# Kernel tuning notes

Measured on AMD Instinct MI355X. Metric: run time of the kernel, lower is better.

Reference implementation:

```python
import jax, jax.numpy as jnp
import numpy as np

N, IN_DIM, OUT_DIM, HEADS = 50000, 128, 32, 8
E = 800000
F = OUT_DIM * HEADS  # 256 fused output features
SEM_HID = 128        # SemanticAttention hidden size (HAN default)


def setup_inputs() -> dict:
    key = jax.random.key(0)
    ks = jax.random.split(key, 16)
    inp = {
        "h": jax.random.normal(ks[0], (N, IN_DIM), jnp.float32),
        "src_a": jax.random.randint(ks[1], (E,), 0, N, jnp.int32),
        "dst_a": jax.random.randint(ks[2], (E,), 0, N, jnp.int32),
        "src_b": jax.random.randint(ks[3], (E,), 0, N, jnp.int32),
        "dst_b": jax.random.randint(ks[4], (E,), 0, N, jnp.int32),
    }
    s = 1.0 / np.sqrt(IN_DIM)
    # per-metapath GATConv params
    inp["W_a"] = jax.random.normal(ks[5], (IN_DIM, F), jnp.float32) * s
    inp["al_a"] = jax.random.normal(ks[6], (HEADS, OUT_DIM), jnp.float32) * 0.1
    inp["ar_a"] = jax.random.normal(ks[7], (HEADS, OUT_DIM), jnp.float32) * 0.1
    inp["bias_a"] = jnp.zeros((F,), jnp.float32)
    inp["W_b"] = jax.random.normal(ks[8], (IN_DIM, F), jnp.float32) * s
    inp["al_b"] = jax.random.normal(ks[9], (HEADS, OUT_DIM), jnp.float32) * 0.1
    inp["ar_b"] = jax.random.normal(ks[10], (HEADS, OUT_DIM), jnp.float32) * 0.1
    inp["bias_b"] = jnp.zeros((F,), jnp.float32)
    # semantic attention params
    inp["Wsem"] = jax.random.normal(ks[11], (F, SEM_HID), jnp.float32) / np.sqrt(F)
    inp["bsem"] = jnp.zeros((SEM_HID,), jnp.float32)
    inp["wsem"] = jax.random.normal(ks[12], (SEM_HID,), jnp.float32) / np.sqrt(SEM_HID)
    return inp


def gat_conv(h, src, dst, W, al, ar, bias):
    # h: [N, in_dim] -> feat: [N, H, D]
    feat = (h @ W).reshape(N, HEADS, OUT_DIM)
    el = (feat * al).sum(-1)  # [N, H]
    er = (feat * ar).sum(-1)  # [N, H]
    e = jax.nn.leaky_relu(el[src] + er[dst], 0.2)  # [E, H]
    # edge softmax over incoming edges of each dst node (numerically stable)
    m = jax.ops.segment_max(e, dst, num_segments=N)        # -inf for empty
    ex = jnp.exp(e - m[dst])                               # [E, H]
    denom = jax.ops.segment_sum(ex, dst, num_segments=N)   # [N, H]
    msg = feat[src] * ex[:, :, None]                       # [E, H, D]
    out = jax.ops.segment_sum(msg, dst, num_segments=N)    # [N, H, D]
    out = out / jnp.where(denom > 0, denom, 1.0)[:, :, None]
    return jax.nn.elu(out.reshape(N, F) + bias)


def reference(h, src_a, dst_a, src_b, dst_b,
              W_a, al_a, ar_a, bias_a,
              W_b, al_b, ar_b, bias_b,
              Wsem, bsem, wsem):
    z_a = gat_conv(h, src_a, dst_a, W_a, al_a, ar_a, bias_a)
    z_b = gat_conv(h, src_b, dst_b, W_b, al_b, ar_b, bias_b)
    z = jnp.stack([z_a, z_b], axis=1)                 # [N, M, F]
    q = jnp.tanh(z @ Wsem + bsem) @ wsem              # [N, M]
    beta = jax.nn.softmax(q.mean(axis=0))             # [M]
    return (z * beta[None, :, None]).sum(axis=1)      # [N, F]
```

## Files before the change

kernel.cpp:

```cpp
#include <hip/hip_runtime.h>
#include <stdint.h>

#define NN 50000
#define EE 800000
#define IN_DIM 128
#define OUT_DIM 32
#define HEADS 8
#define FF 256
#define SH 128
#define NPAD 50048
#define FEXT 272
#define CAP 64

#define RANK_G   6250
#define A_WSEMT0 6250
#define A_BTA0   (A_WSEMT0 + 128)
#define A_BTB0   (A_BTA0 + FEXT)
#define A_G      (A_BTB0 + FEXT)

#define GEMM_BLKS 782
#define B_G      (2 * GEMM_BLKS)

#define PULL_G   12500
#define C_G      (2 * PULL_G)
#define D_G      (2 * GEMM_BLKS)

typedef short s16x8 __attribute__((ext_vector_type(8)));
typedef float f32x4 __attribute__((ext_vector_type(4)));

__device__ __forceinline__ float b2f(unsigned short u) {
    union { unsigned int i; float f; } v; v.i = ((unsigned int)u) << 16; return v.f;
}
__device__ __forceinline__ unsigned short f2b(float f) {
    union { float f; unsigned int i; } v; v.f = f;
    unsigned int i = v.i;
    unsigned int r = (i + 0x7FFFu + ((i >> 16) & 1u)) >> 16;
    return (unsigned short)r;
}

__device__ __forceinline__ void buildBT_one(
    const float* __restrict__ W, const float* __restrict__ al,
    const float* __restrict__ ar, unsigned short* __restrict__ BT,
    int fp, int k)
{
    float v;
    if (fp < FF) {
        v = W[(size_t)k * FF + fp];
    } else if (fp < FF + 8) {
        int hh = fp - FF;
        float s = 0.f;
        #pragma unroll
        for (int d = 0; d < 32; ++d) s += W[(size_t)k * FF + hh * 32 + d] * al[hh * 32 + d];
        v = s;
    } else {
        int hh = fp - FF - 8;
        float s = 0.f;
        #pragma unroll
        for (int d = 0; d < 32; ++d) s += W[(size_t)k * FF + hh * 32 + d] * ar[hh * 32 + d];
        v = s;
    }
    BT[(size_t)fp * IN_DIM + k] = f2b(v);
}

__global__ __launch_bounds__(256) void megaA(
    const int* __restrict__ src_a, const int* __restrict__ dst_a,
    const int* __restrict__ src_b, const int* __restrict__ dst_b,
    int* __restrict__ counts_a, int* __restrict__ counts_b,
    unsigned short* __restrict__ perm_a, unsigned short* __restrict__ perm_b,
    const float* __restrict__ Wsem, unsigned short* __restrict__ WsemT,
    const float* __restrict__ W_a, const float* __restrict__ al_a,
    const float* __restrict__ ar_a, unsigned short* __restrict__ BT_a,
    const float* __restrict__ W_b, const float* __restrict__ al_b,
    const float* __restrict__ ar_b, unsigned short* __restrict__ BT_b)
{
    int b = blockIdx.x, t = threadIdx.x;
    if (b < RANK_G) {
        int idx = b * 256 + t;
        if (idx < EE) {
            int d = dst_a[idx];
            int r = atomicAdd(&counts_a[d], 1);
            perm_a[d * CAP + r] = (unsigned short)src_a[idx];
        } else {
            int e = idx - EE;
            int d = dst_b[e];
            int r = atomicAdd(&counts_b[d], 1);
            perm_b[d * CAP + r] = (unsigned short)src_b[e];
        }
    } else if (b < A_BTA0) {
        int j = b - A_WSEMT0;
        WsemT[j * FF + t] = f2b(Wsem[(size_t)t * SH + j]);
    } else if (b < A_BTB0) {
        if (t < IN_DIM) buildBT_one(W_a, al_a, ar_a, BT_a, b - A_BTA0, t);
    } else {
        if (t < IN_DIM) buildBT_one(W_b, al_b, ar_b, BT_b, b - A_BTB0, t);
    }
}

__global__ __launch_bounds__(256) void megaB(
    const float* __restrict__ h,
    const unsigned short* __restrict__ BT_a, const unsigned short* __restrict__ BT_b,
    unsigned short* __restrict__ feat_a, unsigned short* __restrict__ feat_b,
    float* __restrict__ el_a, float* __restrict__ er_a,
    float* __restrict__ el_b, float* __restrict__ er_b)
{
    int g = blockIdx.x, t = threadIdx.x;
    int mp = (g >= GEMM_BLKS);
    int gb = mp ? g - GEMM_BLKS : g;
    const unsigned short* BT = mp ? BT_b : BT_a;
    unsigned short* feat = mp ? feat_b : feat_a;
    float* el = mp ? el_b : el_a;
    float* er = mp ? er_b : er_a;

    int wave = t >> 6, lane = t & 63;
    int quad = lane >> 4, l16 = lane & 15;
    int nbase = gb * 64 + wave * 16;
    int n = nbase + l16;
    int nr = (n < NN) ? n : (NN - 1);
    const float* hrow = h + (size_t)nr * IN_DIM + quad * 8;
    s16x8 nfr[4];
    #pragma unroll
    for (int kt = 0; kt < 4; ++kt) {
        float4 p0 = *(const float4*)(hrow + kt * 32);
        float4 p1 = *(const float4*)(hrow + kt * 32 + 4);
        s16x8 v;
        v[0] = (short)f2b(p0.x); v[1] = (short)f2b(p0.y);
        v[2] = (short)f2b(p0.z); v[3] = (short)f2b(p0.w);
        v[4] = (short)f2b(p1.x); v[5] = (short)f2b(p1.y);
        v[6] = (short)f2b(p1.z); v[7] = (short)f2b(p1.w);
        nfr[kt] = v;
    }
    bool live = (n < NN);
    #pragma unroll 1
    for (int ft = 0; ft < 17; ++ft) {
        const unsigned short* brow = BT + (size_t)(ft * 16 + l16) * IN_DIM + quad * 8;
        f32x4 c = {0.f, 0.f, 0.f, 0.f};
        #pragma unroll
        for (int kt = 0; kt < 4; ++kt) {
            s16x8 ffr = *(const s16x8*)(brow + kt * 32);
            c = __builtin_amdgcn_mfma_f32_16x16x32_bf16(ffr, nfr[kt], c, 0, 0, 0);
        }
        if (ft < 16) {
            if (live) {
                ushort4 r;
                r.x = f2b(c[0]); r.y = f2b(c[1]); r.z = f2b(c[2]); r.w = f2b(c[3]);
                *(ushort4*)(feat + (size_t)n * FF + ft * 16 + quad * 4) = r;
            }
        } else if (live) {
            #pragma unroll
            for (int r = 0; r < 4; ++r) {
                int jp = quad * 4 + r;
                if (jp < 8) el[n * HEADS + jp] = c[r];
                else        er[n * HEADS + (jp - 8)] = c[r];
            }
        }
    }
}

__global__ __launch_bounds__(256) void megaC(
    const int* __restrict__ counts_a, const int* __restrict__ counts_b,
    const unsigned short* __restrict__ perm_a, const unsigned short* __restrict__ perm_b,
    const float* __restrict__ el_a, const float* __restrict__ er_a,
    const float* __restrict__ el_b, const float* __restrict__ er_b,
    const unsigned short* __restrict__ feat_a, const unsigned short* __restrict__ feat_b,
    const float* __restrict__ bias_a, const float* __restrict__ bias_b,
    unsigned short* __restrict__ zb_a, unsigned short* __restrict__ zb_b)
{
    int bb = blockIdx.x;
    int mp = (bb >= PULL_G);
    int blk = mp ? bb - PULL_G : bb;
    const int* counts = mp ? counts_b : counts_a;
    const unsigned short* perm = mp ? perm_b : perm_a;
    const float* el = mp ? el_b : el_a;
    const float* er = mp ? er_b : er_a;
    const unsigned short* feat = mp ? feat_b : feat_a;
    const float* bias = mp ? bias_b : bias_a;
    unsigned short* zb = mp ? zb_b : zb_a;

    int wave = threadIdx.x >> 6;
    int lane = threadIdx.x & 63;
    int n = blk * 4 + wave;
    int sub = lane >> 5;
    int l32 = lane & 31;
    int head = l32 >> 2;
    int fbase = l32 * 8;
    int deg = counts[n];
    int base = n * CAP;
    float ern = er[n * HEADS + head];
    float den = 0.f;
    float acc[8];
    #pragma unroll
    for (int u = 0; u < 8; ++u) acc[u] = 0.f;

#define STEP(S) {                                                    \
        float x = el[(S) * HEADS + head] + ern;                      \
        x = fmaxf(x, 0.2f * x);                                      \
        float ex = __expf(x);                                        \
        den += ex;                                                   \
        uint4 fv = *(const uint4*)(feat + (size_t)(S) * FF + fbase); \
        const unsigned short* fp = (const unsigned short*)&fv;       \
        acc[0] += b2f(fp[0]) * ex; acc[1] += b2f(fp[1]) * ex;        \
        acc[2] += b2f(fp[2]) * ex; acc[3] += b2f(fp[3]) * ex;        \
        acc[4] += b2f(fp[4]) * ex; acc[5] += b2f(fp[5]) * ex;        \
        acc[6] += b2f(fp[6]) * ex; acc[7] += b2f(fp[7]) * ex; }

    int jp = sub;
    for (; jp + 2 < deg; jp += 4) {
        int s0 = perm[base + jp];
        int s1 = perm[base + jp + 2];
        STEP(s0); STEP(s1);
    }
    if (jp < deg) {
        int s0 = perm[base + jp];
        STEP(s0);
    }
#undef STEP

    den += __shfl_xor(den, 32, 64);
    #pragma unroll
    for (int u = 0; u < 8; ++u) acc[u] += __shfl_xor(acc[u], 32, 64);

    if (den <= 0.f) den = 1.f;
    float inv = 1.f / den;
    float4 b0 = *(const float4*)(bias + fbase);
    float4 b1 = *(const float4*)(bias + fbase + 4);
    float bv[8] = {b0.x, b0.y, b0.z, b0.w, b1.x, b1.y, b1.z, b1.w};
    if (sub == 0) {
        ushort4 r0, r1;
        unsigned short rr[8];
        #pragma unroll
        for (int u = 0; u < 8; ++u) {
            float ov = acc[u] * inv + bv[u];
            ov = (ov > 0.f) ? ov : (__expf(ov) - 1.f);
            rr[u] = f2b(ov);
        }
        r0.x = rr[0]; r0.y = rr[1]; r0.z = rr[2]; r0.w = rr[3];
        r1.x = rr[4]; r1.y = rr[5]; r1.z = rr[6]; r1.w = rr[7];
        *(ushort4*)(zb + (size_t)n * FF + fbase) = r0;
        *(ushort4*)(zb + (size_t)n * FF + fbase + 4) = r1;
    }
}

__global__ __launch_bounds__(256) void megaD(
    const unsigned short* __restrict__ zb_a, const unsigned short* __restrict__ zb_b,
    const unsigned short* __restrict__ WsemT,
    const float* __restrict__ bsem, const float* __restrict__ wsem,
    float* __restrict__ qsum)
{
    int bb = blockIdx.x;
    int mp = (bb >= GEMM_BLKS);
    int blk = mp ? bb - GEMM_BLKS : bb;
    const unsigned short* zb = mp ? zb_b : zb_a;

    int wave = threadIdx.x >> 6, lane = threadIdx.x & 63;
    int quad = lane >> 4, l16 = lane & 15;
    int nbase = blk * 64 + wave * 16;
    const unsigned short* arow = zb + (size_t)(nbase + l16) * FF + quad * 8;
    s16x8 afr[8];
    #pragma unroll
    for (int kt = 0; kt < 8; ++kt)
        afr[kt] = *(const s16x8*)(arow + kt * 32);
    float qacc = 0.f;
    for (int jt = 0; jt < 8; ++jt) {
        int jj = jt * 16 + l16;
        const unsigned short* brow = WsemT + (size_t)jj * FF + quad * 8;
        f32x4 c = {0.f, 0.f, 0.f, 0.f};
        #pragma unroll
        for (int kt = 0; kt < 8; ++kt) {
            s16x8 bfr = *(const s16x8*)(brow + kt * 32);
            c = __builtin_amdgcn_mfma_f32_16x16x32_bf16(afr[kt], bfr, c, 0, 0, 0);
        }
        float bj = bsem[jj], wj = wsem[jj];
        #pragma unroll
        for (int r = 0; r < 4; ++r) {
            int n = nbase + quad * 4 + r;
            float tv = tanhf(c[r] + bj) * wj;
            qacc += (n < NN) ? tv : 0.f;
        }
    }
    #pragma unroll
    for (int o = 1; o < 64; o <<= 1) qacc += __shfl_xor(qacc, o, 64);
    __shared__ float wsum[4];
    if (lane == 0) wsum[wave] = qacc;
    __syncthreads();
    if (threadIdx.x == 0)
        atomicAdd(&qsum[mp], wsum[0] + wsum[1] + wsum[2] + wsum[3]);
}

__global__ __launch_bounds__(256) void combine_kernel(
    const unsigned short* __restrict__ za,
    const unsigned short* __restrict__ zbm,
    float* __restrict__ out, const float* __restrict__ qsum)
{
    size_t i = (size_t)blockIdx.x * blockDim.x + threadIdx.x;
    size_t base = i * 4;
    if (base >= (size_t)NN * FF) return;
    float qa = qsum[0] * (1.f / NN), qb = qsum[1] * (1.f / NN);
    float mx = fmaxf(qa, qb);
    float ea = __expf(qa - mx), eb = __expf(qb - mx);
    float inv = 1.f / (ea + eb);
    float b0 = ea * inv, b1 = eb * inv;
    ushort4 va = *(const ushort4*)(za + base);
    ushort4 vb = *(const ushort4*)(zbm + base);
    float4 r;
    r.x = b0 * b2f(va.x) + b1 * b2f(vb.x);
    r.y = b0 * b2f(va.y) + b1 * b2f(vb.y);
    r.z = b0 * b2f(va.z) + b1 * b2f(vb.z);
    r.w = b0 * b2f(va.w) + b1 * b2f(vb.w);
    *(float4*)(out + base) = r;
}

extern "C" void kernel_launch(void* const* d_in, const int* in_sizes, int n_in,
                              void* d_out, int out_size, void* d_ws, size_t ws_size,
                              hipStream_t stream)
{
    const float* h      = (const float*)d_in[0];
    const int* src_a    = (const int*)d_in[1];
    const int* dst_a    = (const int*)d_in[2];
    const int* src_b    = (const int*)d_in[3];
    const int* dst_b    = (const int*)d_in[4];
    const float* W_a    = (const float*)d_in[5];
    const float* al_a   = (const float*)d_in[6];
    const float* ar_a   = (const float*)d_in[7];
    const float* bias_a = (const float*)d_in[8];
    const float* W_b    = (const float*)d_in[9];
    const float* al_b   = (const float*)d_in[10];
    const float* ar_b   = (const float*)d_in[11];
    const float* bias_b = (const float*)d_in[12];
    const float* Wsem   = (const float*)d_in[13];
    const float* bsem   = (const float*)d_in[14];
    const float* wsem   = (const float*)d_in[15];
    float* out = (float*)d_out;

    char* ws = (char*)d_ws;
    size_t o = 0;
    auto alloc = [&](size_t bytes) -> char* {
        char* p = ws + o;
        o += (bytes + 255) & ~(size_t)255;
        return p;
    };
    unsigned short* BT_a   = (unsigned short*)alloc((size_t)FEXT * IN_DIM * 2);
    unsigned short* BT_b   = (unsigned short*)alloc((size_t)FEXT * IN_DIM * 2);
    unsigned short* feat_a = (unsigned short*)alloc((size_t)NN * FF * 2);
    unsigned short* feat_b = (unsigned short*)alloc((size_t)NN * FF * 2);
    unsigned short* zb_a   = (unsigned short*)alloc((size_t)NPAD * FF * 2);
    unsigned short* zb_b   = (unsigned short*)alloc((size_t)NPAD * FF * 2);
    unsigned short* WsemT  = (unsigned short*)alloc((size_t)SH * FF * 2);
    float* el_a    = (float*)alloc((size_t)NN * HEADS * 4);
    float* er_a    = (float*)alloc((size_t)NN * HEADS * 4);
    float* el_b    = (float*)alloc((size_t)NN * HEADS * 4);
    float* er_b    = (float*)alloc((size_t)NN * HEADS * 4);
    unsigned short* perm_a = (unsigned short*)alloc((size_t)NN * CAP * 2);
    unsigned short* perm_b = (unsigned short*)alloc((size_t)NN * CAP * 2);
    char* zspan0   = ws + o;
    int* counts_a  = (int*)alloc((size_t)NN * 4);
    int* counts_b  = (int*)alloc((size_t)NN * 4);
    float* qsum    = (float*)alloc(8);
    size_t zspan   = (size_t)((ws + o) - zspan0);

    hipMemsetAsync(zspan0, 0, zspan, stream);
    megaA<<<A_G, 256, 0, stream>>>(src_a, dst_a, src_b, dst_b,
                                   counts_a, counts_b, perm_a, perm_b,
                                   Wsem, WsemT,
                                   W_a, al_a, ar_a, BT_a,
                                   W_b, al_b, ar_b, BT_b);
    megaB<<<B_G, 256, 0, stream>>>(h, BT_a, BT_b, feat_a, feat_b,
                                   el_a, er_a, el_b, er_b);
    megaC<<<C_G, 256, 0, stream>>>(counts_a, counts_b, perm_a, perm_b,
                                   el_a, er_a, el_b, er_b,
                                   feat_a, feat_b, bias_a, bias_b, zb_a, zb_b);
    megaD<<<D_G, 256, 0, stream>>>(zb_a, zb_b, WsemT, bsem, wsem, qsum);
    combine_kernel<<<(int)(((size_t)NN * FF / 4 + 255) / 256), 256, 0, stream>>>(zb_a, zb_b, out, qsum);
}
```

Baseline: 494.1 us.

## Split edge bucketing into rank atomics and a scatter pass fused with GEMM

The atomic counting pass now only records each edge's rank within its destination bucket. The scatter of source indices into the per-destination perm table moves into the GEMM kernel as extra blocks, which also clamp writes to CAP. The aim is to shorten the latency-bound atomic kernel and overlap the scattered perm writes with the feature GEMM. In exchange it adds a rank buffer, a second pass over dst/src, and caps degree at CAP in the pull kernel.

```diff
diff --git a/kernel.cpp b/kernel.cpp
--- a/kernel.cpp
+++ b/kernel.cpp
@@ -18,8 +18,9 @@
 #define A_BTB0   (A_BTA0 + FEXT)
 #define A_G      (A_BTB0 + FEXT)
 
+#define B_FILL   6250
 #define GEMM_BLKS 782
-#define B_G      (2 * GEMM_BLKS)
+#define B_G      (B_FILL + 2 * GEMM_BLKS)
 
 #define PULL_G   12500
 #define C_G      (2 * PULL_G)
@@ -63,10 +64,9 @@
 }
 
 __global__ __launch_bounds__(256) void megaA(
-    const int* __restrict__ src_a, const int* __restrict__ dst_a,
-    const int* __restrict__ src_b, const int* __restrict__ dst_b,
+    const int* __restrict__ dst_a, const int* __restrict__ dst_b,
     int* __restrict__ counts_a, int* __restrict__ counts_b,
-    unsigned short* __restrict__ perm_a, unsigned short* __restrict__ perm_b,
+    unsigned short* __restrict__ rank_a, unsigned short* __restrict__ rank_b,
     const float* __restrict__ Wsem, unsigned short* __restrict__ WsemT,
     const float* __restrict__ W_a, const float* __restrict__ al_a,
     const float* __restrict__ ar_a, unsigned short* __restrict__ BT_a,
@@ -77,14 +77,10 @@
     if (b < RANK_G) {
         int idx = b * 256 + t;
         if (idx < EE) {
-            int d = dst_a[idx];
-            int r = atomicAdd(&counts_a[d], 1);
-            perm_a[d * CAP + r] = (unsigned short)src_a[idx];
+            rank_a[idx] = (unsigned short)atomicAdd(&counts_a[dst_a[idx]], 1);
         } else {
             int e = idx - EE;
-            int d = dst_b[e];
-            int r = atomicAdd(&counts_b[d], 1);
-            perm_b[d * CAP + r] = (unsigned short)src_b[e];
+            rank_b[e] = (unsigned short)atomicAdd(&counts_b[dst_b[e]], 1);
         }
     } else if (b < A_BTA0) {
         int j = b - A_WSEMT0;
@@ -97,13 +93,30 @@
 }
 
 __global__ __launch_bounds__(256) void megaB(
+    const int* __restrict__ src_a, const int* __restrict__ dst_a,
+    const int* __restrict__ src_b, const int* __restrict__ dst_b,
+    const unsigned short* __restrict__ rank_a, const unsigned short* __restrict__ rank_b,
+    unsigned short* __restrict__ perm_a, unsigned short* __restrict__ perm_b,
     const float* __restrict__ h,
     const unsigned short* __restrict__ BT_a, const unsigned short* __restrict__ BT_b,
     unsigned short* __restrict__ feat_a, unsigned short* __restrict__ feat_b,
     float* __restrict__ el_a, float* __restrict__ er_a,
     float* __restrict__ el_b, float* __restrict__ er_b)
 {
-    int g = blockIdx.x, t = threadIdx.x;
+    int b = blockIdx.x, t = threadIdx.x;
+    if (b < B_FILL) {
+        int idx = b * 256 + t;
+        if (idx < EE) {
+            int r = rank_a[idx];
+            if (r < CAP) perm_a[dst_a[idx] * CAP + r] = (unsigned short)src_a[idx];
+        } else {
+            int e = idx - EE;
+            int r = rank_b[e];
+            if (r < CAP) perm_b[dst_b[e] * CAP + r] = (unsigned short)src_b[e];
+        }
+        return;
+    }
+    int g = b - B_FILL;
     int mp = (g >= GEMM_BLKS);
     int gb = mp ? g - GEMM_BLKS : g;
     const unsigned short* BT = mp ? BT_b : BT_a;
@@ -184,6 +197,7 @@
     int head = l32 >> 2;
     int fbase = l32 * 8;
     int deg = counts[n];
+    if (deg > CAP) deg = CAP;
     int base = n * CAP;
     float ern = er[n * HEADS + head];
     float den = 0.f;
@@ -349,6 +363,8 @@
     float* er_a    = (float*)alloc((size_t)NN * HEADS * 4);
     float* el_b    = (float*)alloc((size_t)NN * HEADS * 4);
     float* er_b    = (float*)alloc((size_t)NN * HEADS * 4);
+    unsigned short* rank_a = (unsigned short*)alloc((size_t)EE * 2);
+    unsigned short* rank_b = (unsigned short*)alloc((size_t)EE * 2);
     unsigned short* perm_a = (unsigned short*)alloc((size_t)NN * CAP * 2);
     unsigned short* perm_b = (unsigned short*)alloc((size_t)NN * CAP * 2);
     char* zspan0   = ws + o;
@@ -358,12 +374,13 @@
     size_t zspan   = (size_t)((ws + o) - zspan0);
 
     hipMemsetAsync(zspan0, 0, zspan, stream);
-    megaA<<<A_G, 256, 0, stream>>>(src_a, dst_a, src_b, dst_b,
-                                   counts_a, counts_b, perm_a, perm_b,
+    megaA<<<A_G, 256, 0, stream>>>(dst_a, dst_b, counts_a, counts_b, rank_a, rank_b,
                                    Wsem, WsemT,
                                    W_a, al_a, ar_a, BT_a,
                                    W_b, al_b, ar_b, BT_b);
-    megaB<<<B_G, 256, 0, stream>>>(h, BT_a, BT_b, feat_a, feat_b,
+    megaB<<<B_G, 256, 0, stream>>>(src_a, dst_a, src_b, dst_b,
+                                   rank_a, rank_b, perm_a, perm_b,
+                                   h, BT_a, BT_b, feat_a, feat_b,
                                    el_a, er_a, el_b, er_b);
     megaC<<<C_G, 256, 0, stream>>>(counts_a, counts_b, perm_a, perm_b,
                                    el_a, er_a, el_b, er_b,
```

Measured after the change: 471.1 us. 4.7% less time.

## Fuse pipeline stages into one cooperative persistent kernel with grid syncs

Applied to the files above, without the earlier changes.

Replaces the chain of separate launches (rank/prep, GEMM, pull, semantic, combine) with a single cooperative kernel of 1024 persistent blocks that loops over virtual blocks and uses grid.sync between phases. The edge bucketing now runs concurrently with the GEMM phase, and bucket overflow is guarded by clamping to CAP. The aim is to remove launch gaps and kernel-boundary drains, at the cost of grid-wide barrier overhead, a fixed grid size that may under-occupy phases, and reduced latency hiding in the memory-bound pull phase. A non-cooperative multi-kernel fallback is kept.

```diff
diff --git a/kernel.cpp b/kernel.cpp
--- a/kernel.cpp
+++ b/kernel.cpp
@@ -1,8 +1,12 @@
 #include <hip/hip_runtime.h>
+#include <hip/hip_cooperative_groups.h>
 #include <stdint.h>
+
+namespace cg = cooperative_groups;
 
 #define NN 50000
 #define EE 800000
+#define EHALF 400000
 #define IN_DIM 128
 #define OUT_DIM 32
 #define HEADS 8
@@ -12,18 +16,11 @@
 #define FEXT 272
 #define CAP 64
 
-#define RANK_G   6250
-#define A_WSEMT0 6250
-#define A_BTA0   (A_WSEMT0 + 128)
-#define A_BTB0   (A_BTA0 + FEXT)
-#define A_G      (A_BTB0 + FEXT)
-
+#define CGRID 1024
+#define RANKC 1563
 #define GEMM_BLKS 782
-#define B_G      (2 * GEMM_BLKS)
-
-#define PULL_G   12500
-#define C_G      (2 * PULL_G)
-#define D_G      (2 * GEMM_BLKS)
+#define PULL_G 12500
+#define PREP_V 672
 
 typedef short s16x8 __attribute__((ext_vector_type(8)));
 typedef float f32x4 __attribute__((ext_vector_type(4)));
@@ -37,6 +34,20 @@
     unsigned int r = (i + 0x7FFFu + ((i >> 16) & 1u)) >> 16;
     return (unsigned short)r;
 }
+
+struct KParams {
+    const int *src_a, *dst_a, *src_b, *dst_b;
+    const float *h;
+    const float *W_a, *al_a, *ar_a, *bias_a;
+    const float *W_b, *al_b, *ar_b, *bias_b;
+    const float *Wsem, *bsem, *wsem;
+    float* out;
+    unsigned short *BT_a, *BT_b, *feat_a, *feat_b, *zb_a, *zb_b, *WsemT;
+    float *el_a, *er_a, *el_b, *er_b;
+    unsigned short *perm_a, *perm_b;
+    int *counts_a, *counts_b;
+    float *qsum;
+};
 
 __device__ __forceinline__ void buildBT_one(
     const float* __restrict__ W, const float* __restrict__ al,
@@ -62,55 +73,46 @@
     BT[(size_t)fp * IN_DIM + k] = f2b(v);
 }
 
-__global__ __launch_bounds__(256) void megaA(
-    const int* __restrict__ src_a, const int* __restrict__ dst_a,
-    const int* __restrict__ src_b, const int* __restrict__ dst_b,
-    int* __restrict__ counts_a, int* __restrict__ counts_b,
-    unsigned short* __restrict__ perm_a, unsigned short* __restrict__ perm_b,
-    const float* __restrict__ Wsem, unsigned short* __restrict__ WsemT,
-    const float* __restrict__ W_a, const float* __restrict__ al_a,
-    const float* __restrict__ ar_a, unsigned short* __restrict__ BT_a,
-    const float* __restrict__ W_b, const float* __restrict__ al_b,
-    const float* __restrict__ ar_b, unsigned short* __restrict__ BT_b)
+__device__ __forceinline__ void dev_prep(const KParams& p, int vb, int t) {
+    if (vb < 128) {
+        p.WsemT[vb * FF + t] = f2b(p.Wsem[(size_t)t * SH + vb]);
+    } else if (vb < 128 + FEXT) {
+        if (t < IN_DIM) buildBT_one(p.W_a, p.al_a, p.ar_a, p.BT_a, vb - 128, t);
+    } else {
+        if (t < IN_DIM) buildBT_one(p.W_b, p.al_b, p.ar_b, p.BT_b, vb - 128 - FEXT, t);
+    }
+}
+
+__device__ __forceinline__ void dev_rank4(const KParams& p, int vb, int t) {
+    int e0 = vb * 256 + t;
+    int e1 = e0 + EHALF;
+    if (e0 < EHALF) {
+        int d = p.dst_a[e0];
+        int r = atomicAdd(&p.counts_a[d], 1);
+        if (r < CAP) p.perm_a[d * CAP + r] = (unsigned short)p.src_a[e0];
+    }
+    if (e1 < EE) {
+        int d = p.dst_a[e1];
+        int r = atomicAdd(&p.counts_a[d], 1);
+        if (r < CAP) p.perm_a[d * CAP + r] = (unsigned short)p.src_a[e1];
+    }
+    if (e0 < EHALF) {
+        int d = p.dst_b[e0];
+        int r = atomicAdd(&p.counts_b[d], 1);
+        if (r < CAP) p.perm_b[d * CAP + r] = (unsigned short)p.src_b[e0];
+    }
+    if (e1 < EE) {
+        int d = p.dst_b[e1];
+        int r = atomicAdd(&p.counts_b[d], 1);
+        if (r < CAP) p.perm_b[d * CAP + r] = (unsigned short)p.src_b[e1];
+    }
+}
+
+__device__ __forceinline__ void dev_gemm(
+    int gb, int t, const float* __restrict__ h,
+    const unsigned short* __restrict__ BT, unsigned short* __restrict__ feat,
+    float* __restrict__ el, float* __restrict__ er)
 {
-    int b = blockIdx.x, t = threadIdx.x;
-    if (b < RANK_G) {
-        int idx = b * 256 + t;
-        if (idx < EE) {
-            int d = dst_a[idx];
-            int r = atomicAdd(&counts_a[d], 1);
-            perm_a[d * CAP + r] = (unsigned short)src_a[idx];
-        } else {
-            int e = idx - EE;
-            int d = dst_b[e];
-            int r = atomicAdd(&counts_b[d], 1);
-            perm_b[d * CAP + r] = (unsigned short)src_b[e];
-        }
-    } else if (b < A_BTA0) {
-        int j = b - A_WSEMT0;
-        WsemT[j * FF + t] = f2b(Wsem[(size_t)t * SH + j]);
-    } else if (b < A_BTB0) {
-        if (t < IN_DIM) buildBT_one(W_a, al_a, ar_a, BT_a, b - A_BTA0, t);
-    } else {
-        if (t < IN_DIM) buildBT_one(W_b, al_b, ar_b, BT_b, b - A_BTB0, t);
-    }
-}
-
-__global__ __launch_bounds__(256) void megaB(
-    const float* __restrict__ h,
-    const unsigned short* __restrict__ BT_a, const unsigned short* __restrict__ BT_b,
-    unsigned short* __restrict__ feat_a, unsigned short* __restrict__ feat_b,
-    float* __restrict__ el_a, float* __restrict__ er_a,
-    float* __restrict__ el_b, float* __restrict__ er_b)
-{
-    int g = blockIdx.x, t = threadIdx.x;
-    int mp = (g >= GEMM_BLKS);
-    int gb = mp ? g - GEMM_BLKS : g;
-    const unsigned short* BT = mp ? BT_b : BT_a;
-    unsigned short* feat = mp ? feat_b : feat_a;
-    float* el = mp ? el_b : el_a;
-    float* er = mp ? er_b : er_a;
-
     int wave = t >> 6, lane = t & 63;
     int quad = lane >> 4, l16 = lane & 15;
     int nbase = gb * 64 + wave * 16;
@@ -156,34 +158,22 @@
     }
 }
 
-__global__ __launch_bounds__(256) void megaC(
-    const int* __restrict__ counts_a, const int* __restrict__ counts_b,
-    const unsigned short* __restrict__ perm_a, const unsigned short* __restrict__ perm_b,
-    const float* __restrict__ el_a, const float* __restrict__ er_a,
-    const float* __restrict__ el_b, const float* __restrict__ er_b,
-    const unsigned short* __restrict__ feat_a, const unsigned short* __restrict__ feat_b,
-    const float* __restrict__ bias_a, const float* __restrict__ bias_b,
-    unsigned short* __restrict__ zb_a, unsigned short* __restrict__ zb_b)
+__device__ __forceinline__ void dev_pull(
+    int blk, int tid,
+    const int* __restrict__ counts, const unsigned short* __restrict__ perm,
+    const float* __restrict__ el, const float* __restrict__ er,
+    const unsigned short* __restrict__ feat, const float* __restrict__ bias,
+    unsigned short* __restrict__ zb)
 {
-    int bb = blockIdx.x;
-    int mp = (bb >= PULL_G);
-    int blk = mp ? bb - PULL_G : bb;
-    const int* counts = mp ? counts_b : counts_a;
-    const unsigned short* perm = mp ? perm_b : perm_a;
-    const float* el = mp ? el_b : el_a;
-    const float* er = mp ? er_b : er_a;
-    const unsigned short* feat = mp ? feat_b : feat_a;
-    const float* bias = mp ? bias_b : bias_a;
-    unsigned short* zb = mp ? zb_b : zb_a;
-
-    int wave = threadIdx.x >> 6;
-    int lane = threadIdx.x & 63;
+    int wave = tid >> 6;
+    int lane = tid & 63;
     int n = blk * 4 + wave;
     int sub = lane >> 5;
     int l32 = lane & 31;
     int head = l32 >> 2;
     int fbase = l32 * 8;
     int deg = counts[n];
+    if (deg > CAP) deg = CAP;
     int base = n * CAP;
     float ern = er[n * HEADS + head];
     float den = 0.f;
@@ -240,18 +230,14 @@
     }
 }
 
-__global__ __launch_bounds__(256) void megaD(
-    const unsigned short* __restrict__ zb_a, const unsigned short* __restrict__ zb_b,
+__device__ __forceinline__ void dev_sem(
+    int blk, int tid, const unsigned short* __restrict__ zb,
     const unsigned short* __restrict__ WsemT,
     const float* __restrict__ bsem, const float* __restrict__ wsem,
-    float* __restrict__ qsum)
+    float* __restrict__ qsum, int idx)
 {
-    int bb = blockIdx.x;
-    int mp = (bb >= GEMM_BLKS);
-    int blk = mp ? bb - GEMM_BLKS : bb;
-    const unsigned short* zb = mp ? zb_b : zb_a;
-
-    int wave = threadIdx.x >> 6, lane = threadIdx.x & 63;
+    __shared__ float wsum[4];
+    int wave = tid >> 6, lane = tid & 63;
     int quad = lane >> 4, l16 = lane & 15;
     int nbase = blk * 64 + wave * 16;
     const unsigned short* arow = zb + (size_t)(nbase + l16) * FF + quad * 8;
@@ -279,95 +265,172 @@
     }
     #pragma unroll
     for (int o = 1; o < 64; o <<= 1) qacc += __shfl_xor(qacc, o, 64);
-    __shared__ float wsum[4];
     if (lane == 0) wsum[wave] = qacc;
     __syncthreads();
-    if (threadIdx.x == 0)
-        atomicAdd(&qsum[mp], wsum[0] + wsum[1] + wsum[2] + wsum[3]);
-}
-
-__global__ __launch_bounds__(256) void combine_kernel(
-    const unsigned short* __restrict__ za,
-    const unsigned short* __restrict__ zbm,
-    float* __restrict__ out, const float* __restrict__ qsum)
-{
+    if (tid == 0)
+        atomicAdd(&qsum[idx], wsum[0] + wsum[1] + wsum[2] + wsum[3]);
+    __syncthreads();
+}
+
+__global__ __launch_bounds__(256, 4) void coop_kernel(KParams p) {
+    cg::grid_group grid = cg::this_grid();
+    const int b0 = blockIdx.x, t = threadIdx.x;
+
+    for (int vb = b0; vb < PREP_V; vb += CGRID) dev_prep(p, vb, t);
+    grid.sync();
+
+    for (int vb = b0; vb < RANKC + 2 * GEMM_BLKS; vb += CGRID) {
+        if (vb < RANKC) {
+            dev_rank4(p, vb, t);
+        } else {
+            int g = vb - RANKC;
+            int mp = (g >= GEMM_BLKS);
+            int gb = mp ? g - GEMM_BLKS : g;
+            dev_gemm(gb, t, p.h, mp ? p.BT_b : p.BT_a, mp ? p.feat_b : p.feat_a,
+                     mp ? p.el_b : p.el_a, mp ? p.er_b : p.er_a);
+        }
+    }
+    grid.sync();
+
+    for (int vb = b0; vb < 2 * PULL_G; vb += CGRID) {
+        int mp = (vb >= PULL_G);
+        int blk = mp ? vb - PULL_G : vb;
+        dev_pull(blk, t, mp ? p.counts_b : p.counts_a, mp ? p.perm_b : p.perm_a,
+                 mp ? p.el_b : p.el_a, mp ? p.er_b : p.er_a,
+                 mp ? p.feat_b : p.feat_a, mp ? p.bias_b : p.bias_a,
+                 mp ? p.zb_b : p.zb_a);
+    }
+    grid.sync();
+
+    for (int vb = b0; vb < 2 * GEMM_BLKS; vb += CGRID) {
+        int mp = (vb >= GEMM_BLKS);
+        int blk = mp ? vb - GEMM_BLKS : vb;
+        dev_sem(blk, t, mp ? p.zb_b : p.zb_a, p.WsemT, p.bsem, p.wsem, p.qsum, mp);
+    }
+    grid.sync();
+
+    float qa = p.qsum[0] * (1.f / NN), qb = p.qsum[1] * (1.f / NN);
+    float mx = fmaxf(qa, qb);
+    float ea = __expf(qa - mx), eb = __expf(qb - mx);
+    float inv = 1.f / (ea + eb);
+    float w0 = ea * inv, w1 = eb * inv;
+    for (size_t i = (size_t)b0 * 256 + t; i < (size_t)NN * FF / 4; i += (size_t)CGRID * 256) {
+        size_t base = i * 4;
+        ushort4 va = *(const ushort4*)(p.zb_a + base);
+        ushort4 vb4 = *(const ushort4*)(p.zb_b + base);
+        float4 r;
+        r.x = w0 * b2f(va.x) + w1 * b2f(vb4.x);
+        r.y = w0 * b2f(va.y) + w1 * b2f(vb4.y);
+        r.z = w0 * b2f(va.z) + w1 * b2f(vb4.z);
+        r.w = w0 * b2f(va.w) + w1 * b2f(vb4.w);
+        *(float4*)(p.out + base) = r;
+    }
+}
+
+__global__ __launch_bounds__(256) void k_prep_rank(KParams p) {
+    int b = blockIdx.x, t = threadIdx.x;
+    if (b < RANKC) dev_rank4(p, b, t);
+    else dev_prep(p, b - RANKC, t);
+}
+__global__ __launch_bounds__(256) void k_gemm(KParams p) {
+    int g = blockIdx.x, t = threadIdx.x;
+    int mp = (g >= GEMM_BLKS);
+    int gb = mp ? g - GEMM_BLKS : g;
+    dev_gemm(gb, t, p.h, mp ? p.BT_b : p.BT_a, mp ? p.feat_b : p.feat_a,
+             mp ? p.el_b : p.el_a, mp ? p.er_b : p.er_a);
+}
+__global__ __launch_bounds__(256) void k_pull(KParams p) {
+    int bb = blockIdx.x, t = threadIdx.x;
+    int mp = (bb >= PULL_G);
+    int blk = mp ? bb - PULL_G : bb;
+    dev_pull(blk, t, mp ? p.counts_b : p.counts_a, mp ? p.perm_b : p.perm_a,
+             mp ? p.el_b : p.el_a, mp ? p.er_b : p.er_a,
+             mp ? p.feat_b : p.feat_a, mp ? p.bias_b : p.bias_a,
+             mp ? p.zb_b : p.zb_a);
+}
+__global__ __launch_bounds__(256) void k_sem(KParams p) {
+    int bb = blockIdx.x, t = threadIdx.x;
+    int mp = (bb >= GEMM_BLKS);
+    int blk = mp ? bb - GEMM_BLKS : bb;
+    dev_sem(blk, t, mp ? p.zb_b : p.zb_a, p.WsemT, p.bsem, p.wsem, p.qsum, mp);
+}
+__global__ __launch_bounds__(256) void k_combine(KParams p) {
     size_t i = (size_t)blockIdx.x * blockDim.x + threadIdx.x;
     size_t base = i * 4;
     if (base >= (size_t)NN * FF) return;
-    float qa = qsum[0] * (1.f / NN), qb = qsum[1] * (1.f / NN);
+    float qa = p.qsum[0] * (1.f / NN), qb = p.qsum[1] * (1.f / NN);
     float mx = fmaxf(qa, qb);
     float ea = __expf(qa - mx), eb = __expf(qb - mx);
     float inv = 1.f / (ea + eb);
-    float b0 = ea * inv, b1 = eb * inv;
-    ushort4 va = *(const ushort4*)(za + base);
-    ushort4 vb = *(const ushort4*)(zbm + base);
+    float w0 = ea * inv, w1 = eb * inv;
+    ushort4 va = *(const ushort4*)(p.zb_a + base);
+    ushort4 vb4 = *(const ushort4*)(p.zb_b + base);
     float4 r;
-    r.x = b0 * b2f(va.x) + b1 * b2f(vb.x);
-    r.y = b0 * b2f(va.y) + b1 * b2f(vb.y);
-    r.z = b0 * b2f(va.z) + b1 * b2f(vb.z);
-    r.w = b0 * b2f(va.w) + b1 * b2f(vb.w);
-    *(float4*)(out + base) = r;
+    r.x = w0 * b2f(va.x) + w1 * b2f(vb4.x);
+    r.y = w0 * b2f(va.y) + w1 * b2f(vb4.y);
+    r.z = w0 * b2f(va.z) + w1 * b2f(vb4.z);
+    r.w = w0 * b2f(va.w) + w1 * b2f(vb4.w);
+    *(float4*)(p.out + base) = r;
 }
 
 extern "C" void kernel_launch(void* const* d_in, const int* in_sizes, int n_in,
                               void* d_out, int out_size, void* d_ws, size_t ws_size,
                               hipStream_t stream)
 {
-    const float* h      = (const float*)d_in[0];
-    const int* src_a    = (const int*)d_in[1];
-    const int* dst_a    = (const int*)d_in[2];
-    const int* src_b    = (const int*)d_in[3];
-    const int* dst_b    = (const int*)d_in[4];
-    const float* W_a    = (const float*)d_in[5];
-    const float* al_a   = (const float*)d_in[6];
-    const float* ar_a   = (const float*)d_in[7];
-    const float* bias_a = (const float*)d_in[8];
-    const float* W_b    = (const float*)d_in[9];
-    const float* al_b   = (const float*)d_in[10];
-    const float* ar_b   = (const float*)d_in[11];
-    const float* bias_b = (const float*)d_in[12];
-    const float* Wsem   = (const float*)d_in[13];
-    const float* bsem   = (const float*)d_in[14];
-    const float* wsem   = (const float*)d_in[15];
-    float* out = (float*)d_out;
+    KParams p;
+    p.h      = (const float*)d_in[0];
+    p.src_a  = (const int*)d_in[1];
+    p.dst_a  = (const int*)d_in[2];
+    p.src_b  = (const int*)d_in[3];
+    p.dst_b  = (const int*)d_in[4];
+    p.W_a    = (const float*)d_in[5];
+    p.al_a   = (const float*)d_in[6];
+    p.ar_a   = (const float*)d_in[7];
+    p.bias_a = (const float*)d_in[8];
+    p.W_b    = (const float*)d_in[9];
+    p.al_b   = (const float*)d_in[10];
+    p.ar_b   = (const float*)d_in[11];
+    p.bias_b = (const float*)d_in[12];
+    p.Wsem   = (const float*)d_in[13];
+    p.bsem   = (const float*)d_in[14];
+    p.wsem   = (const float*)d_in[15];
+    p.out    = (float*)d_out;
 
     char* ws = (char*)d_ws;
     size_t o = 0;
     auto alloc = [&](size_t bytes) -> char* {
-        char* p = ws + o;
+        char* pq = ws + o;
         o += (bytes + 255) & ~(size_t)255;
-        return p;
+        return pq;
     };
-    unsigned short* BT_a   = (unsigned short*)alloc((size_t)FEXT * IN_DIM * 2);
-    unsigned short* BT_b   = (unsigned short*)alloc((size_t)FEXT * IN_DIM * 2);
-    unsigned short* feat_a = (unsigned short*)alloc((size_t)NN * FF * 2);
-    unsigned short* feat_b = (unsigned short*)alloc((size_t)NN * FF * 2);
-    unsigned short* zb_a   = (unsigned short*)alloc((size_t)NPAD * FF * 2);
-    unsigned short* zb_b   = (unsigned short*)alloc((size_t)NPAD * FF * 2);
-    unsigned short* WsemT  = (unsigned short*)alloc((size_t)SH * FF * 2);
-    float* el_a    = (float*)alloc((size_t)NN * HEADS * 4);
-    float* er_a    = (float*)alloc((size_t)NN * HEADS * 4);
-    float* el_b    = (float*)alloc((size_t)NN * HEADS * 4);
-    float* er_b    = (float*)alloc((size_t)NN * HEADS * 4);
-    unsigned short* perm_a = (unsigned short*)alloc((size_t)NN * CAP * 2);
-    unsigned short* perm_b = (unsigned short*)alloc((size_t)NN * CAP * 2);
-    char* zspan0   = ws + o;
-    int* counts_a  = (int*)alloc((size_t)NN * 4);
-    int* counts_b  = (int*)alloc((size_t)NN * 4);
-    float* qsum    = (float*)alloc(8);
-    size_t zspan   = (size_t)((ws + o) - zspan0);
-
-    hipMemsetAsync(zspan0, 0, zspan, stream);
-    megaA<<<A_G, 256, 0, stream>>>(src_a, dst_a, src_b, dst_b,
-                                   counts_a, counts_b, perm_a, perm_b,
-                                   Wsem, WsemT,
-                                   W_a, al_a, ar_a, BT_a,
-                                   W_b, al_b, ar_b, BT_b);
-    megaB<<<B_G, 256, 0, stream>>>(h, BT_a, BT_b, feat_a, feat_b,
-                                   el_a, er_a, el_b, er_b);
-    megaC<<<C_G, 256, 0, stream>>>(counts_a, counts_b, perm_a, perm_b,
-                                   el_a, er_a, el_b, er_b,
-                                   feat_a, feat_b, bias_a, bias_b, zb_a, zb_b);
-    megaD<<<D_G, 256, 0, stream>>>(zb_a, zb_b, WsemT, bsem, wsem, qsum);
-    combine_kernel<<<(int)(((size_t)NN * FF / 4 + 255) / 256), 256, 0, stream>>>(zb_a, zb_b, out, qsum);
-}
+    p.BT_a   = (unsigned short*)alloc((size_t)FEXT * IN_DIM * 2);
+    p.BT_b   = (unsigned short*)alloc((size_t)FEXT * IN_DIM * 2);
+    p.feat_a = (unsigned short*)alloc((size_t)NN * FF * 2);
+    p.feat_b = (unsigned short*)alloc((size_t)NN * FF * 2);
+    p.zb_a   = (unsigned short*)alloc((size_t)NPAD * FF * 2);
+    p.zb_b   = (unsigned short*)alloc((size_t)NPAD * FF * 2);
+    p.WsemT  = (unsigned short*)alloc((size_t)SH * FF * 2);
+    p.el_a   = (float*)alloc((size_t)NN * HEADS * 4);
+    p.er_a   = (float*)alloc((size_t)NN * HEADS * 4);
+    p.el_b   = (float*)alloc((size_t)NN * HEADS * 4);
+    p.er_b   = (float*)alloc((size_t)NN * HEADS * 4);
+    p.perm_a = (unsigned short*)alloc((size_t)NN * CAP * 2);
+    p.perm_b = (unsigned short*)alloc((size_t)NN * CAP * 2);
+    int* zero_base = (int*)alloc(((size_t)2 * NN + 2) * 4);
+    p.counts_a = zero_base;
+    p.counts_b = zero_base + NN;
+    p.qsum     = (float*)(zero_base + 2 * NN);
+
+    hipMemsetAsync(zero_base, 0, ((size_t)2 * NN + 2) * 4, stream);
+
+    void* args[] = { (void*)&p };
+    hipError_t err = hipLaunchCooperativeKernel(
+        (const void*)coop_kernel, dim3(CGRID), dim3(256), args, 0, stream);
+    if (err != hipSuccess) {
+        k_prep_rank<<<RANKC + PREP_V, 256, 0, stream>>>(p);
+        k_gemm<<<2 * GEMM_BLKS, 256, 0, stream>>>(p);
+        k_pull<<<2 * PULL_G, 256, 0, stream>>>(p);
+        k_sem<<<2 * GEMM_BLKS, 256, 0, stream>>>(p);
+        k_combine<<<(int)(((size_t)NN * FF / 4 + 255) / 256), 256, 0, stream>>>(p);
+    }
+}
```

After: 1.032 ms. +109.0%, slower.
